# Kernel optimization log

Measured on AMD Instinct MI355X. Metric: run time of the kernel, lower is better.

## Reference

```python
import jax, jax.numpy as jnp
import numpy as np

W_DIM, T_DIM = 300, 100
IN = W_DIM + T_DIM        # 400, also LSTM hidden size
H = IN                    # hiddenSize
BI = 2 * H                # 800, biLSTM output per step
MLP_IN = 2 * BI           # 1600
VOCAB, NTAGS = 50000, 50
SEQ = 320


def _lstm_dir(xs, w_ih, w_hh, b_ih, b_hh, h0, c0, reverse):
    # xs: [T, d_in]; PyTorch gate order i, f, g, o
    if reverse:
        xs = xs[::-1]
    def step(carry, x):
        h, c = carry
        g = x @ w_ih.T + h @ w_hh.T + b_ih + b_hh
        i, f, gc, o = jnp.split(g, 4)
        i, f, o = jax.nn.sigmoid(i), jax.nn.sigmoid(f), jax.nn.sigmoid(o)
        c = f * c + i * jnp.tanh(gc)
        h = o * jnp.tanh(c)
        return (h, c), h
    _, ys = jax.lax.scan(step, (h0, c0), xs)
    return ys[::-1] if reverse else ys


def _bilstm(x, params, h0, c0):
    # x: [T, IN]; h0/c0: [4, H] ordered (l0 fwd, l0 bwd, l1 fwd, l1 bwd)
    out = x
    for layer in range(2):
        p_f = params[layer][0]
        p_b = params[layer][1]
        yf = _lstm_dir(out, *p_f, h0[2 * layer],     c0[2 * layer],     False)
        yb = _lstm_dir(out, *p_b, h0[2 * layer + 1], c0[2 * layer + 1], True)
        out = jnp.concatenate([yf, yb], axis=-1)  # [T, 2H]
    return out


def setup_inputs() -> dict:
    key = jax.random.key(0)
    ks = iter(jax.random.split(key, 32))
    inp = {}
    inp['words'] = jax.random.randint(next(ks), (SEQ,), 0, VOCAB)
    inp['tags'] = jax.random.randint(next(ks), (SEQ,), 0, NTAGS)
    inp['arcs'] = jax.random.randint(next(ks), (SEQ + 1,), 0, SEQ + 1)
    inp['word_emb'] = jax.random.normal(next(ks), (VOCAB, W_DIM), jnp.float32) * 0.1
    inp['tag_emb'] = jax.random.normal(next(ks), (NTAGS, T_DIM), jnp.float32) * 0.1
    inp['h0'] = jax.random.normal(next(ks), (4, H), jnp.float32)
    inp['c0'] = jax.random.normal(next(ks), (4, H), jnp.float32)
    s = 1.0 / np.sqrt(H)
    for layer, d_in in ((0, IN), (1, BI)):
        for suf in ('', 'r'):
            inp[f'w_ih_l{layer}{suf}'] = jax.random.uniform(next(ks), (4 * H, d_in), jnp.float32, -s, s)
            inp[f'w_hh_l{layer}{suf}'] = jax.random.uniform(next(ks), (4 * H, H), jnp.float32, -s, s)
            inp[f'b_ih_l{layer}{suf}'] = jax.random.uniform(next(ks), (4 * H,), jnp.float32, -s, s)
            inp[f'b_hh_l{layer}{suf}'] = jax.random.uniform(next(ks), (4 * H,), jnp.float32, -s, s)
    inp['mlp_w1'] = jax.random.normal(next(ks), (MLP_IN, MLP_IN), jnp.float32) * 0.02
    inp['mlp_b1'] = jnp.zeros((MLP_IN,), jnp.float32)
    inp['mlp_w2'] = jax.random.normal(next(ks), (1, MLP_IN), jnp.float32) * 0.02
    inp['mlp_b2'] = jnp.zeros((1,), jnp.float32)
    return inp


def reference(words, tags, arcs, word_emb, tag_emb, h0, c0,
              w_ih_l0, w_hh_l0, b_ih_l0, b_hh_l0,
              w_ih_l0r, w_hh_l0r, b_ih_l0r, b_hh_l0r,
              w_ih_l1, w_hh_l1, b_ih_l1, b_hh_l1,
              w_ih_l1r, w_hh_l1r, b_ih_l1r, b_hh_l1r,
              mlp_w1, mlp_b1, mlp_w2, mlp_b2):
    n = words.shape[0]
    x = jnp.concatenate([word_emb[words], tag_emb[tags]], axis=1)  # [n, IN]
    params = (((w_ih_l0, w_hh_l0, b_ih_l0, b_hh_l0), (w_ih_l0r, w_hh_l0r, b_ih_l0r, b_hh_l0r)),
              ((w_ih_l1, w_hh_l1, b_ih_l1, b_hh_l1), (w_ih_l1r, w_hh_l1r, b_ih_l1r, b_hh_l1r)))
    hv = _bilstm(x, params, h0, c0)  # [n, BI]
    # pairwise MLP: concat(h_head, h_dep) @ W1.T == h_head @ W1a.T + h_dep @ W1b.T
    w1a, w1b = mlp_w1[:, :BI], mlp_w1[:, BI:]
    a = hv @ w1a.T  # [n, MLP_IN], head part
    b = hv @ w1b.T  # [n, MLP_IN], dep part
    hid = jax.nn.relu(a[:, None, :] + b[None, :, :] + mlp_b1)  # [n, n, MLP_IN]
    scores = jnp.einsum('ndk,ok->nd', hid, mlp_w2)[..., 0] if mlp_w2.shape[0] != 1 else (hid @ mlp_w2[0] + mlp_b2[0])  # [n, n]
    offdiag = 1.0 - jnp.eye(n, dtype=scores.dtype)
    score_tensor = jnp.zeros((n + 1, n + 1), scores.dtype)
    score_tensor = score_tensor.at[0, 0].set(1.0)
    score_tensor = score_tensor.at[1:, 1:].set(scores * offdiag)
    return score_tensor
```

## Files before the change

### kernel.cpp

```cpp
#include <hip/hip_runtime.h>
#include <hip/hip_bf16.h>
#include <hip/hip_fp16.h>

#define SEQ   320
#define GATES 1600
#define NCOL  3200
#define GDW   25
#define RPW   16

typedef _Float16 half2v __attribute__((ext_vector_type(2)));
typedef _Float16 f16x8  __attribute__((ext_vector_type(8)));
typedef float    f32x4  __attribute__((ext_vector_type(4)));
union H2U { unsigned u; half2v h; __half2 hh; };

__global__ __launch_bounds__(256) void prep_kernel(
    const int* __restrict__ words, const int* __restrict__ tags,
    const float* __restrict__ wemb, const float* __restrict__ temb,
    _Float16* __restrict__ Ah0,
    const float* __restrict__ bihl0,  const float* __restrict__ bhhl0,
    const float* __restrict__ bihl0r, const float* __restrict__ bhhl0r,
    const float* __restrict__ bihl1,  const float* __restrict__ bhhl1,
    const float* __restrict__ bihl1r, const float* __restrict__ bhhl1r,
    const float* __restrict__ mlpb1,
    float* __restrict__ bL0, float* __restrict__ bL1, float* __restrict__ bAB,
    const float* __restrict__ wih0, const float* __restrict__ wih0r,
    _Float16* __restrict__ BhA)
{
    const int b = blockIdx.x, t = threadIdx.x;
    if (b < 520) {
        int i = b * 256 + t;
        if (i >= SEQ * 416) return;
        int tt = i / 416, c = i % 416;
        float v = 0.f;
        if (c < 300)      v = wemb[(size_t)words[tt] * 300 + c];
        else if (c < 400) v = temb[(size_t)tags[tt] * 100 + (c - 300)];
        Ah0[i] = (_Float16)v;
    } else if (b < 533) {
        int g = (b - 520) * 256 + t;
        if (g >= NCOL) return;
        if (g < GATES) {
            bL0[g] = bihl0[g] + bhhl0[g];
            bL1[g] = bihl1[g] + bhhl1[g];
            bAB[g] = mlpb1[g];
        } else {
            int q = g - GATES;
            bL0[g] = bihl0r[q] + bhhl0r[q];
            bL1[g] = bihl1r[q] + bhhl1r[q];
            bAB[g] = 0.f;
        }
    } else {
        int i = (b - 533) * 256 + t;
        if (i >= NCOL * 416) return;
        int n = i / 416, k = i % 416;
        float v = 0.f;
        if (k < 400)
            v = (n < GATES) ? wih0[(size_t)n * 400 + k]
                            : wih0r[(size_t)(n - GATES) * 400 + k];
        BhA[i] = (_Float16)v;
    }
}

__global__ __launch_bounds__(256) void cvt2_kernel(
    const float* __restrict__ wih1, const float* __restrict__ wih1r,
    _Float16* __restrict__ BhB,
    const float* __restrict__ mlpw1, _Float16* __restrict__ BhA)
{
    const int b = blockIdx.x, t = threadIdx.x;
    if (b < 10000) {
        int i = b * 256 + t;
        if (i >= NCOL * 800) return;
        int n = i / 800, k = i % 800;
        BhB[i] = (_Float16)((n < GATES) ? wih1[(size_t)n * 800 + k]
                                        : wih1r[(size_t)(n - GATES) * 800 + k]);
    } else {
        int i = (b - 10000) * 256 + t;
        if (i >= NCOL * 800) return;
        int n = i / 800, k = i % 800;
        BhA[i] = (_Float16)((n < GATES) ? mlpw1[(size_t)n * 1600 + k]
                                        : mlpw1[(size_t)(n - GATES) * 1600 + 800 + k]);
    }
}

__global__ __launch_bounds__(256) void gemm_f16(
    const _Float16* __restrict__ A, int Kp,
    const _Float16* __restrict__ B,
    const float* __restrict__ bias, float* __restrict__ C)
{
    const int tid  = threadIdx.x;
    const int w    = tid >> 6, lane = tid & 63;
    const int quad = lane >> 4, l16 = lane & 15;
    const int mb   = blockIdx.y * 32 + (w & 1) * 16;
    const int n0   = blockIdx.x * 64 + (w >> 1) * 32;
    const _Float16* Arow = A + (size_t)(mb + l16) * Kp + quad * 8;
    const _Float16* B0r  = B + (size_t)(n0 + l16) * Kp + quad * 8;
    const _Float16* B1r  = B0r + (size_t)16 * Kp;
    f32x4 acc0 = {0.f, 0.f, 0.f, 0.f}, acc1 = {0.f, 0.f, 0.f, 0.f};
#pragma unroll 4
    for (int k0 = 0; k0 < Kp; k0 += 32) {
        f16x8 a  = *(const f16x8*)(Arow + k0);
        f16x8 b0 = *(const f16x8*)(B0r + k0);
        f16x8 b1 = *(const f16x8*)(B1r + k0);
        acc0 = __builtin_amdgcn_mfma_f32_16x16x32_f16(a, b0, acc0, 0, 0, 0);
        acc1 = __builtin_amdgcn_mfma_f32_16x16x32_f16(a, b1, acc1, 0, 0, 0);
    }
    const int mr = mb + quad * 4;
    float bn0 = bias[n0 + l16], bn1 = bias[n0 + 16 + l16];
#pragma unroll
    for (int r = 0; r < 4; ++r) {
        C[(size_t)(mr + r) * NCOL + n0 + l16]      = acc0[r] + bn0;
        C[(size_t)(mr + r) * NCOL + n0 + 16 + l16] = acc1[r] + bn1;
    }
}

__global__ __launch_bounds__(256) void lstm_layer(
    const float* __restrict__ gates,
    const float* __restrict__ whh_f, const float* __restrict__ whh_b,
    const float* __restrict__ h0f, const float* __restrict__ h0b,
    const float* __restrict__ c0f, const float* __restrict__ c0b,
    unsigned* __restrict__ ex,
    _Float16* __restrict__ ah)
{
    __shared__ __align__(16) unsigned hbuf[2][224];
    const int tid = threadIdx.x;
    const int dir = blockIdx.x >= GDW;
    const int wg  = blockIdx.x - dir * GDW;
    const float* whh = dir ? whh_b : whh_f;
    const float* h0d = dir ? h0b : h0f;
    const float* c0d = dir ? c0b : c0f;

    const int rp = tid >> 5;
    const int g  = (tid >> 3) & 3;
    const int ks = tid & 7;
    const int jA = wg * RPW + 2 * rp;

    unsigned wrA[25], wrB[25];
    {
        const float2* wA = (const float2*)(whh + ((size_t)g * 400 + jA) * 400 + 50 * ks);
        const float2* wB = (const float2*)(whh + ((size_t)g * 400 + jA + 1) * 400 + 50 * ks);
#pragma unroll
        for (int i = 0; i < 25; ++i) {
            float2 fa = wA[i], fb = wB[i];
            H2U ca, cbu;
            ca.hh  = __floats2half2_rn(fa.x, fa.y);
            cbu.hh = __floats2half2_rn(fb.x, fb.y);
            wrA[i] = ca.u; wrB[i] = cbu.u;
        }
    }

    int bp = 0, pollq = 0;
    if (tid < 192) {
        bp = tid >> 3; bp += (bp >= wg);
        int q = bp * 8 + (tid & 7);
        pollq = (q / 25) * 28 + q % 25;
    }
    const int qown    = wg * 8 + rp;
    const int ownaddr = (qown / 25) * 28 + qown % 25;
    const float* gbase = gates + dir * GATES + g * 400 + jA;
    unsigned* exq = ex + ((size_t)(dir * GDW + wg) * SEQ) * 16 + rp;
    unsigned* ahq = (unsigned*)ah + dir * 200 + wg * 8 + rp;

    float cA = c0d[jA], cB = c0d[jA + 1];

    for (int s = 0; s < SEQ; ++s) {
        const int row = dir ? (SEQ - 1 - s) : s;
        const int cb  = s & 1;
        float2 gv = *(const float2*)(gbase + (size_t)row * NCOL);

        if (s == 0) {
            if (tid < 200) {
                float2 f = ((const float2*)h0d)[tid];
                H2U a; a.hh = __floats2half2_rn(f.x, f.y);
                hbuf[0][(tid / 25) * 28 + tid % 25] = a.u;
            }
        } else if (tid < 192) {
            const int rprev = dir ? row + 1 : row - 1;
            const unsigned* src = ex + (((size_t)dir * GDW + bp) * SEQ + rprev) * 16 + (tid & 7);
            unsigned v;
            do {
                v = __hip_atomic_load(src, __ATOMIC_RELAXED, __HIP_MEMORY_SCOPE_AGENT);
            } while (v == 0xFFFFFFFFu);
            hbuf[cb][pollq] = v;
        }
        __syncthreads();

        const unsigned* hb = &hbuf[cb][ks * 28];
        float accA = 0.f, accB = 0.f;
#pragma unroll
        for (int i = 0; i < 6; ++i) {
            uint4 hq = *(const uint4*)(hb + 4 * i);
            H2U x0, x1, x2, x3, wa, wb;
            x0.u = hq.x; x1.u = hq.y; x2.u = hq.z; x3.u = hq.w;
            wa.u = wrA[4*i+0]; wb.u = wrB[4*i+0];
            accA = __builtin_amdgcn_fdot2(wa.h, x0.h, accA, false);
            accB = __builtin_amdgcn_fdot2(wb.h, x0.h, accB, false);
            wa.u = wrA[4*i+1]; wb.u = wrB[4*i+1];
            accA = __builtin_amdgcn_fdot2(wa.h, x1.h, accA, false);
            accB = __builtin_amdgcn_fdot2(wb.h, x1.h, accB, false);
            wa.u = wrA[4*i+2]; wb.u = wrB[4*i+2];
            accA = __builtin_amdgcn_fdot2(wa.h, x2.h, accA, false);
            accB = __builtin_amdgcn_fdot2(wb.h, x2.h, accB, false);
            wa.u = wrA[4*i+3]; wb.u = wrB[4*i+3];
            accA = __builtin_amdgcn_fdot2(wa.h, x3.h, accA, false);
            accB = __builtin_amdgcn_fdot2(wb.h, x3.h, accB, false);
        }
        {
            H2U xl, wa, wb; xl.u = hb[24];
            wa.u = wrA[24]; wb.u = wrB[24];
            accA = __builtin_amdgcn_fdot2(wa.h, xl.h, accA, false);
            accB = __builtin_amdgcn_fdot2(wb.h, xl.h, accB, false);
        }

        accA += __shfl_xor(accA, 1); accA += __shfl_xor(accA, 2); accA += __shfl_xor(accA, 4);
        accB += __shfl_xor(accB, 1); accB += __shfl_xor(accB, 2); accB += __shfl_xor(accB, 4);
        accA += gv.x; accB += gv.y;

        float a1 = __shfl_xor(accA, 8), a2 = __shfl_xor(accA, 16), a3 = __shfl_xor(accA, 24);
        float b1 = __shfl_xor(accB, 8), b2 = __shfl_xor(accB, 16), b3 = __shfl_xor(accB, 24);
        float giA = g==0?accA : g==1?a1 : g==2?a2 : a3;
        float gfA = g==1?accA : g==0?a1 : g==3?a2 : a3;
        float ggA = g==2?accA : g==3?a1 : g==0?a2 : a3;
        float goA = g==3?accA : g==2?a1 : g==1?a2 : a3;
        float giB = g==0?accB : g==1?b1 : g==2?b2 : b3;
        float gfB = g==1?accB : g==0?b1 : g==3?b2 : b3;
        float ggB = g==2?accB : g==3?b1 : g==0?b2 : b3;
        float goB = g==3?accB : g==2?b1 : g==1?b2 : b3;

        float ivA = 1.f / (1.f + __expf(-giA)), fvA = 1.f / (1.f + __expf(-gfA));
        float ovA = 1.f / (1.f + __expf(-goA)), tgA = 1.f - 2.f / (1.f + __expf(2.f * ggA));
        float ivB = 1.f / (1.f + __expf(-giB)), fvB = 1.f / (1.f + __expf(-gfB));
        float ovB = 1.f / (1.f + __expf(-goB)), tgB = 1.f - 2.f / (1.f + __expf(2.f * ggB));
        cA = fvA * cA + ivA * tgA;
        cB = fvB * cB + ivB * tgB;
        float hA = ovA * (1.f - 2.f / (1.f + __expf(2.f * cA)));
        float hB = ovB * (1.f - 2.f / (1.f + __expf(2.f * cB)));

        if ((tid & 31) == 0) {
            H2U pk; pk.hh = __floats2half2_rn(hA, hB);
            __hip_atomic_store(exq + (size_t)row * 16, pk.u,
                               __ATOMIC_RELAXED, __HIP_MEMORY_SCOPE_AGENT);
            ahq[(size_t)row * 400] = pk.u;
            hbuf[cb ^ 1][ownaddr] = pk.u;
        }
    }
}

__global__ __launch_bounds__(256) void scores_kernel(
    const float* __restrict__ ab, const float* __restrict__ w2,
    const float* __restrict__ b2, float* __restrict__ out)
{
    if (blockIdx.y == 20) {
        int i = blockIdx.x * 256 + threadIdx.y * 16 + threadIdx.x;
        if (blockIdx.x < 2 && i < 321) {
            out[i]               = (i == 0) ? 1.f : 0.f;
            out[(size_t)i * 321] = (i == 0) ? 1.f : 0.f;
        }
        return;
    }
    __shared__ float a_s[16 * 132];
    __shared__ float b_s[16 * 132];
    __shared__ float w_s[128];
    const int tx = threadIdx.x, ty = threadIdx.y;
    const int tid = ty * 16 + tx;
    const int n0 = blockIdx.y * 16, d0 = blockIdx.x * 16;
    float acc = 0.f;
    for (int kc = 0; kc < 1600; kc += 128) {
        for (int i = tid; i < 16 * 128; i += 256) {
            int r = i >> 7, c = i & 127;
            a_s[r * 132 + c] = ab[(size_t)(n0 + r) * NCOL + kc + c];
            b_s[r * 132 + c] = ab[(size_t)(d0 + r) * NCOL + 1600 + kc + c];
        }
        if (tid < 128) w_s[tid] = w2[kc + tid];
        __syncthreads();
#pragma unroll
        for (int k = 0; k < 128; k += 4) {
            float4 av = *(const float4*)&a_s[ty * 132 + k];
            float4 bv = *(const float4*)&b_s[tx * 132 + k];
            float4 wv = *(const float4*)&w_s[k];
            acc += fmaxf(av.x + bv.x, 0.f) * wv.x;
            acc += fmaxf(av.y + bv.y, 0.f) * wv.y;
            acc += fmaxf(av.z + bv.z, 0.f) * wv.z;
            acc += fmaxf(av.w + bv.w, 0.f) * wv.w;
        }
        __syncthreads();
    }
    int n = n0 + ty, d = d0 + tx;
    out[(size_t)(n + 1) * 321 + (d + 1)] = (n == d) ? 0.f : (acc + b2[0]);
}

extern "C" void kernel_launch(void* const* d_in, const int* in_sizes, int n_in,
                              void* d_out, int out_size, void* d_ws, size_t ws_size,
                              hipStream_t stream)
{
    const int*   words    = (const int*)d_in[0];
    const int*   tags     = (const int*)d_in[1];
    const float* wemb     = (const float*)d_in[3];
    const float* temb     = (const float*)d_in[4];
    const float* h0       = (const float*)d_in[5];
    const float* c0       = (const float*)d_in[6];
    const float* w_ih_l0  = (const float*)d_in[7];
    const float* w_hh_l0  = (const float*)d_in[8];
    const float* b_ih_l0  = (const float*)d_in[9];
    const float* b_hh_l0  = (const float*)d_in[10];
    const float* w_ih_l0r = (const float*)d_in[11];
    const float* w_hh_l0r = (const float*)d_in[12];
    const float* b_ih_l0r = (const float*)d_in[13];
    const float* b_hh_l0r = (const float*)d_in[14];
    const float* w_ih_l1  = (const float*)d_in[15];
    const float* w_hh_l1  = (const float*)d_in[16];
    const float* b_ih_l1  = (const float*)d_in[17];
    const float* b_hh_l1  = (const float*)d_in[18];
    const float* w_ih_l1r = (const float*)d_in[19];
    const float* w_hh_l1r = (const float*)d_in[20];
    const float* b_ih_l1r = (const float*)d_in[21];
    const float* b_hh_l1r = (const float*)d_in[22];
    const float* mlp_w1   = (const float*)d_in[23];
    const float* mlp_b1   = (const float*)d_in[24];
    const float* mlp_w2   = (const float*)d_in[25];
    const float* mlp_b2   = (const float*)d_in[26];
    float* out = (float*)d_out;

    float* ws      = (float*)d_ws;
    float*    gates  = ws;
    float*    biasL0 = ws + 1024000;
    float*    biasL1 = ws + 1027200;
    float*    biasAB = ws + 1030400;
    unsigned* ex     = (unsigned*)(ws + 1033600);
    _Float16* Ah0    = (_Float16*)(ws + 1289600);
    _Float16* Ah1    = (_Float16*)(ws + 1356160);
    _Float16* Ah2    = (_Float16*)(ws + 1484160);
    _Float16* BhA    = (_Float16*)(ws + 1612160);
    _Float16* BhB    = (_Float16*)(ws + 2892160);

    hipMemsetAsync(ex, 0xFF, 256000u * 4, stream);

    prep_kernel<<<5733, 256, 0, stream>>>(
        words, tags, wemb, temb, Ah0,
        b_ih_l0, b_hh_l0, b_ih_l0r, b_hh_l0r,
        b_ih_l1, b_hh_l1, b_ih_l1r, b_hh_l1r,
        mlp_b1, biasL0, biasL1, biasAB, w_ih_l0, w_ih_l0r, BhA);

    gemm_f16<<<dim3(50, 10), 256, 0, stream>>>(Ah0, 416, BhA, biasL0, gates);
    cvt2_kernel<<<20000, 256, 0, stream>>>(w_ih_l1, w_ih_l1r, BhB, mlp_w1, BhA);
    lstm_layer<<<2 * GDW, 256, 0, stream>>>(gates, w_hh_l0, w_hh_l0r,
                                            h0, h0 + 400, c0, c0 + 400, ex, Ah1);
    hipMemsetAsync(ex, 0xFF, 256000u * 4, stream);
    gemm_f16<<<dim3(50, 10), 256, 0, stream>>>(Ah1, 800, BhB, biasL1, gates);
    lstm_layer<<<2 * GDW, 256, 0, stream>>>(gates, w_hh_l1, w_hh_l1r,
                                            h0 + 800, h0 + 1200, c0 + 800, c0 + 1200,
                                            ex, Ah2);
    gemm_f16<<<dim3(50, 10), 256, 0, stream>>>(Ah2, 800, BhA, biasAB, gates);

    scores_kernel<<<dim3(20, 21), dim3(16, 16), 0, stream>>>(gates, mlp_w2, mlp_b2, out);
}
```

Measured before the change: 1.458 ms.

## Use fewer, larger LSTM workgroups to cut cross-block h exchange

The recurrent LSTM kernel now runs 5 workgroups of 640 threads per direction instead of 25 of 256. Each thread holds 50 packed weight pairs and splits K four ways instead of eight. Fewer producer blocks means each step polls fewer peers, and the polls and stores use 64-bit words carrying two h pairs, with a lighter barrier. The risks are higher register pressure per thread (launch bounds 640,3) and more serial dot-product work per step on fewer CUs.

```diff
diff --git a/kernel.cpp b/kernel.cpp
--- a/kernel.cpp
+++ b/kernel.cpp
@@ -5,8 +5,9 @@
 #define SEQ   320
 #define GATES 1600
 #define NCOL  3200
-#define GDW   25
-#define RPW   16
+#define GDW   5
+#define RPW   80
+#define EXS   48
 
 typedef _Float16 half2v __attribute__((ext_vector_type(2)));
 typedef _Float16 f16x8  __attribute__((ext_vector_type(8)));
@@ -112,7 +113,7 @@
     }
 }
 
-__global__ __launch_bounds__(256) void lstm_layer(
+__global__ __launch_bounds__(640, 3) void lstm_layer(
     const float* __restrict__ gates,
     const float* __restrict__ whh_f, const float* __restrict__ whh_b,
     const float* __restrict__ h0f, const float* __restrict__ h0b,
@@ -120,7 +121,7 @@
     unsigned* __restrict__ ex,
     _Float16* __restrict__ ah)
 {
-    __shared__ __align__(16) unsigned hbuf[2][224];
+    __shared__ __align__(16) unsigned hbuf[2][208];
     const int tid = threadIdx.x;
     const int dir = blockIdx.x >= GDW;
     const int wg  = blockIdx.x - dir * GDW;
@@ -128,17 +129,17 @@
     const float* h0d = dir ? h0b : h0f;
     const float* c0d = dir ? c0b : c0f;
 
-    const int rp = tid >> 5;
-    const int g  = (tid >> 3) & 3;
-    const int ks = tid & 7;
+    const int rp = tid >> 4;
+    const int g  = (tid >> 2) & 3;
+    const int ks = tid & 3;
     const int jA = wg * RPW + 2 * rp;
 
-    unsigned wrA[25], wrB[25];
+    unsigned wrA[50], wrB[50];
     {
-        const float2* wA = (const float2*)(whh + ((size_t)g * 400 + jA) * 400 + 50 * ks);
-        const float2* wB = (const float2*)(whh + ((size_t)g * 400 + jA + 1) * 400 + 50 * ks);
+        const float2* wA = (const float2*)(whh + ((size_t)g * 400 + jA) * 400 + 100 * ks);
+        const float2* wB = (const float2*)(whh + ((size_t)g * 400 + jA + 1) * 400 + 100 * ks);
 #pragma unroll
-        for (int i = 0; i < 25; ++i) {
+        for (int i = 0; i < 50; ++i) {
             float2 fa = wA[i], fb = wB[i];
             H2U ca, cbu;
             ca.hh  = __floats2half2_rn(fa.x, fa.y);
@@ -147,18 +148,27 @@
         }
     }
 
-    int bp = 0, pollq = 0;
-    if (tid < 192) {
-        bp = tid >> 3; bp += (bp >= wg);
-        int q = bp * 8 + (tid & 7);
-        pollq = (q / 25) * 28 + q % 25;
-    }
-    const int qown    = wg * 8 + rp;
-    const int ownaddr = (qown / 25) * 28 + qown % 25;
+    int pollq0 = 0, pollq1 = 0;
+    const unsigned long long* pbase = nullptr;
+    if (tid < 80) {
+        int pp = tid / 20; pp += (pp >= wg);
+        int u  = tid % 20;
+        int q0 = pp * 40 + 2 * u;
+        pollq0 = (q0 / 50) * 52 + q0 % 50;
+        pollq1 = ((q0 + 1) / 50) * 52 + (q0 + 1) % 50;
+        pbase  = (const unsigned long long*)(ex + ((size_t)(dir * GDW + pp) * SEQ) * EXS + 2 * u);
+    }
+
+    const int w64  = tid >> 6;
+    const int hsel = (tid >> 5) & 1;
+    const int qo   = wg * 40 + 4 * w64 + 2 * hsel;
+    const int own0 = (qo / 50) * 52 + qo % 50;
+    const int own1 = ((qo + 1) / 50) * 52 + (qo + 1) % 50;
+    unsigned long long* exo = (unsigned long long*)(ex + ((size_t)(dir * GDW + wg) * SEQ) * EXS
+                                                    + 4 * w64 + 2 * hsel);
+    unsigned* ahd = (unsigned*)ah;
+    const int ahoff = dir * 200 + wg * 40 + 4 * w64 + 2 * hsel;
     const float* gbase = gates + dir * GATES + g * 400 + jA;
-    unsigned* exq = ex + ((size_t)(dir * GDW + wg) * SEQ) * 16 + rp;
-    unsigned* ahq = (unsigned*)ah + dir * 200 + wg * 8 + rp;
-
     float cA = c0d[jA], cB = c0d[jA + 1];
 
     for (int s = 0; s < SEQ; ++s) {
@@ -167,26 +177,33 @@
         float2 gv = *(const float2*)(gbase + (size_t)row * NCOL);
 
         if (s == 0) {
-            if (tid < 200) {
-                float2 f = ((const float2*)h0d)[tid];
-                H2U a; a.hh = __floats2half2_rn(f.x, f.y);
-                hbuf[0][(tid / 25) * 28 + tid % 25] = a.u;
+            if (tid < 100) {
+                float4 f = ((const float4*)h0d)[tid];
+                H2U a, b;
+                a.hh = __floats2half2_rn(f.x, f.y);
+                b.hh = __floats2half2_rn(f.z, f.w);
+                int q0 = 2 * tid, q1 = 2 * tid + 1;
+                hbuf[0][(q0 / 50) * 52 + q0 % 50] = a.u;
+                hbuf[0][(q1 / 50) * 52 + q1 % 50] = b.u;
             }
-        } else if (tid < 192) {
+        } else if (tid < 80) {
             const int rprev = dir ? row + 1 : row - 1;
-            const unsigned* src = ex + (((size_t)dir * GDW + bp) * SEQ + rprev) * 16 + (tid & 7);
-            unsigned v;
+            const unsigned long long* src = pbase + (size_t)rprev * (EXS / 2);
+            unsigned long long v;
             do {
                 v = __hip_atomic_load(src, __ATOMIC_RELAXED, __HIP_MEMORY_SCOPE_AGENT);
-            } while (v == 0xFFFFFFFFu);
-            hbuf[cb][pollq] = v;
-        }
-        __syncthreads();
-
-        const unsigned* hb = &hbuf[cb][ks * 28];
+            } while (((unsigned)v == 0xFFFFFFFFu) || ((unsigned)(v >> 32) == 0xFFFFFFFFu));
+            hbuf[cb][pollq0] = (unsigned)v;
+            hbuf[cb][pollq1] = (unsigned)(v >> 32);
+        }
+        asm volatile("s_waitcnt lgkmcnt(0)" ::: "memory");
+        __builtin_amdgcn_s_barrier();
+        __builtin_amdgcn_sched_barrier(0);
+
+        const unsigned* hb = &hbuf[cb][ks * 52];
         float accA = 0.f, accB = 0.f;
 #pragma unroll
-        for (int i = 0; i < 6; ++i) {
+        for (int i = 0; i < 12; ++i) {
             uint4 hq = *(const uint4*)(hb + 4 * i);
             H2U x0, x1, x2, x3, wa, wb;
             x0.u = hq.x; x1.u = hq.y; x2.u = hq.z; x3.u = hq.w;
@@ -204,18 +221,23 @@
             accB = __builtin_amdgcn_fdot2(wb.h, x3.h, accB, false);
         }
         {
-            H2U xl, wa, wb; xl.u = hb[24];
-            wa.u = wrA[24]; wb.u = wrB[24];
-            accA = __builtin_amdgcn_fdot2(wa.h, xl.h, accA, false);
-            accB = __builtin_amdgcn_fdot2(wb.h, xl.h, accB, false);
-        }
-
-        accA += __shfl_xor(accA, 1); accA += __shfl_xor(accA, 2); accA += __shfl_xor(accA, 4);
-        accB += __shfl_xor(accB, 1); accB += __shfl_xor(accB, 2); accB += __shfl_xor(accB, 4);
+            uint2 ht = *(const uint2*)(hb + 48);
+            H2U x0, x1, wa, wb;
+            x0.u = ht.x; x1.u = ht.y;
+            wa.u = wrA[48]; wb.u = wrB[48];
+            accA = __builtin_amdgcn_fdot2(wa.h, x0.h, accA, false);
+            accB = __builtin_amdgcn_fdot2(wb.h, x0.h, accB, false);
+            wa.u = wrA[49]; wb.u = wrB[49];
+            accA = __builtin_amdgcn_fdot2(wa.h, x1.h, accA, false);
+            accB = __builtin_amdgcn_fdot2(wb.h, x1.h, accB, false);
+        }
+
+        accA += __shfl_xor(accA, 1); accA += __shfl_xor(accA, 2);
+        accB += __shfl_xor(accB, 1); accB += __shfl_xor(accB, 2);
         accA += gv.x; accB += gv.y;
 
-        float a1 = __shfl_xor(accA, 8), a2 = __shfl_xor(accA, 16), a3 = __shfl_xor(accA, 24);
-        float b1 = __shfl_xor(accB, 8), b2 = __shfl_xor(accB, 16), b3 = __shfl_xor(accB, 24);
+        float a1 = __shfl_xor(accA, 4), a2 = __shfl_xor(accA, 8), a3 = __shfl_xor(accA, 12);
+        float b1 = __shfl_xor(accB, 4), b2 = __shfl_xor(accB, 8), b3 = __shfl_xor(accB, 12);
         float giA = g==0?accA : g==1?a1 : g==2?a2 : a3;
         float gfA = g==1?accA : g==0?a1 : g==3?a2 : a3;
         float ggA = g==2?accA : g==3?a1 : g==0?a2 : a3;
@@ -234,12 +256,15 @@
         float hA = ovA * (1.f - 2.f / (1.f + __expf(2.f * cA)));
         float hB = ovB * (1.f - 2.f / (1.f + __expf(2.f * cB)));
 
+        H2U pk; pk.hh = __floats2half2_rn(hA, hB);
+        unsigned hi = __shfl_xor(pk.u, 16);
         if ((tid & 31) == 0) {
-            H2U pk; pk.hh = __floats2half2_rn(hA, hB);
-            __hip_atomic_store(exq + (size_t)row * 16, pk.u,
+            unsigned long long val = ((unsigned long long)hi << 32) | pk.u;
+            __hip_atomic_store(exo + (size_t)row * (EXS / 2), val,
                                __ATOMIC_RELAXED, __HIP_MEMORY_SCOPE_AGENT);
-            ahq[(size_t)row * 400] = pk.u;
-            hbuf[cb ^ 1][ownaddr] = pk.u;
+            *(uint2*)(ahd + (size_t)row * 400 + ahoff) = make_uint2(pk.u, hi);
+            hbuf[cb ^ 1][own0] = pk.u;
+            hbuf[cb ^ 1][own1] = hi;
         }
     }
 }
@@ -325,13 +350,13 @@
     float*    biasL1 = ws + 1027200;
     float*    biasAB = ws + 1030400;
     unsigned* ex     = (unsigned*)(ws + 1033600);
-    _Float16* Ah0    = (_Float16*)(ws + 1289600);
-    _Float16* Ah1    = (_Float16*)(ws + 1356160);
-    _Float16* Ah2    = (_Float16*)(ws + 1484160);
-    _Float16* BhA    = (_Float16*)(ws + 1612160);
-    _Float16* BhB    = (_Float16*)(ws + 2892160);
-
-    hipMemsetAsync(ex, 0xFF, 256000u * 4, stream);
+    _Float16* Ah0    = (_Float16*)(ws + 1187200);
+    _Float16* Ah1    = (_Float16*)(ws + 1253760);
+    _Float16* Ah2    = (_Float16*)(ws + 1381760);
+    _Float16* BhA    = (_Float16*)(ws + 1509760);
+    _Float16* BhB    = (_Float16*)(ws + 2789760);
+
+    hipMemsetAsync(ex, 0xFF, 153600u * 4, stream);
 
     prep_kernel<<<5733, 256, 0, stream>>>(
         words, tags, wemb, temb, Ah0,
@@ -341,11 +366,11 @@
 
     gemm_f16<<<dim3(50, 10), 256, 0, stream>>>(Ah0, 416, BhA, biasL0, gates);
     cvt2_kernel<<<20000, 256, 0, stream>>>(w_ih_l1, w_ih_l1r, BhB, mlp_w1, BhA);
-    lstm_layer<<<2 * GDW, 256, 0, stream>>>(gates, w_hh_l0, w_hh_l0r,
+    lstm_layer<<<2 * GDW, 640, 0, stream>>>(gates, w_hh_l0, w_hh_l0r,
                                             h0, h0 + 400, c0, c0 + 400, ex, Ah1);
-    hipMemsetAsync(ex, 0xFF, 256000u * 4, stream);
+    hipMemsetAsync(ex, 0xFF, 153600u * 4, stream);
     gemm_f16<<<dim3(50, 10), 256, 0, stream>>>(Ah1, 800, BhB, biasL1, gates);
-    lstm_layer<<<2 * GDW, 256, 0, stream>>>(gates, w_hh_l1, w_hh_l1r,
+    lstm_layer<<<2 * GDW, 640, 0, stream>>>(gates, w_hh_l1, w_hh_l1r,
                                             h0 + 800, h0 + 1200, c0 + 800, c0 + 1200,
                                             ex, Ah2);
     gemm_f16<<<dim3(50, 10), 256, 0, stream>>>(Ah2, 800, BhA, biasAB, gates);
```

Result: slower. 2.109 ms (+44.6%).
